# Optimization experiments

Measured on AMD Instinct MI355X. Metric: run time of the kernel, lower is better.

## Reference

```python
import jax, jax.numpy as jnp
import numpy as np

EPS = 1e-06
NB, NGRID, NTARGET, NBASIS, NCH, OUTCH = 4, 512, 1024, 5, 8, 1


def setup_inputs() -> dict:
    key = jax.random.key(0)
    k1, k2, k3, k4 = jax.random.split(key, 4)
    x_grid = jax.random.normal(k1, (NB, NGRID, NCH), dtype=jnp.float32)
    h_grid = jax.random.normal(k2, (NB, NGRID, NBASIS, NCH), dtype=jnp.float32)
    target_x = jax.random.normal(k3, (NB, NTARGET, NCH), dtype=jnp.float32)
    # sigma initialized as log(min_init_lengthscale + init_lengthscale) = log(1 + 1e-6)
    sigma = jnp.full((NBASIS, NCH), np.log(1e-06 + 1.0), dtype=jnp.float32)
    # linear g: nbasis -> out_channels
    g_w = jax.random.normal(k4, (OUTCH, NBASIS), dtype=jnp.float32) / np.sqrt(NBASIS)
    g_b = jnp.zeros((OUTCH,), dtype=jnp.float32)
    return {"x_grid": x_grid, "h_grid": h_grid, "target_x": target_x,
            "sigma": sigma, "g_w": g_w, "g_b": g_b}


def reference(x_grid, h_grid, target_x, sigma, g_w, g_b):
    # scales: (nbasis, nchannel)
    scales = jnp.exp(sigma) + EPS
    # pairwise scaled distances: (nb, ngrid, ntarget, nbasis, nchannel)
    d = (x_grid[:, :, None, None, :] - target_x[:, None, :, None, :]) / scales[None, None, None, :, :]
    wt = jnp.exp(-0.5 * d * d)
    # weighted sum over grid points: (nb, ntarget, nbasis, nchannel)
    h_out = jnp.einsum('bgkc,bgtkc->btkc', h_grid, wt)
    # transpose to (nb, ntarget, nchannel, nbasis), linear over nbasis
    h_out = jnp.swapaxes(h_out, -2, -1)
    out = jnp.einsum('btck,ok->btco', h_out, g_w) + g_b
    out = jnp.squeeze(out)  # out_channels == 1 -> (nb, ntarget, nchannel)
    if out.ndim == 2:
        out = out[None]
    return out
```

## Files before the change

kernel.cpp:

```cpp
#include <hip/hip_runtime.h>

#define NB 4
#define NGRID 512
#define NTARGET 1024
#define NBASIS 5
#define NCH 8
#define EPS_F 1e-6f
#define LOG2E 1.4426950408889634f

#if defined(__has_builtin)
#if __has_builtin(__builtin_amdgcn_exp2f)
#define EXP2F(x) __builtin_amdgcn_exp2f(x)
#else
#define EXP2F(x) exp2f(x)
#endif
#else
#define EXP2F(x) exp2f(x)
#endif

__global__ __launch_bounds__(256) void final_layer_fused(
    const float* __restrict__ x_grid,
    const float* __restrict__ h_grid,
    const float* __restrict__ target_x,
    const float* __restrict__ sigma,
    const float* __restrict__ g_w,
    const float* __restrict__ g_b,
    float* __restrict__ out)
{
    __shared__ float xs[NGRID * NCH];
    __shared__ float hw[NGRID * NCH];
    __shared__ float coef_s[NBASIS * NCH];
    __shared__ float gw_s[NBASIS];

    const int tid = threadIdx.x;
    const int c   = tid & 7;
    const int tt  = (tid >> 3) & 7;
    const int gs  = tid >> 6;
    const int b   = blockIdx.x >> 7;
    const int t   = ((blockIdx.x & 127) << 3) + tt;

    if (tid < NBASIS * NCH) {
        float s = __expf(sigma[tid]) + EPS_F;
        coef_s[tid] = -0.5f * LOG2E / (s * s);
    }
    if (tid < NBASIS) gw_s[tid] = g_w[tid];

    const float gw0 = g_w[0], gw1 = g_w[1], gw2 = g_w[2], gw3 = g_w[3], gw4 = g_w[4];
    const float* xbase = x_grid + (size_t)b * NGRID * NCH;
    const float* hbase = h_grid + (size_t)b * NGRID * NBASIS * NCH;
#pragma unroll
    for (int j = 0; j < 16; ++j) {
        const int v = tid + j * 256;
        xs[v] = xbase[v];
        const float* hp = hbase + (size_t)(v >> 3) * (NBASIS * NCH) + (v & 7);
        hw[v] = gw0 * hp[0] + gw1 * hp[8] + gw2 * hp[16] + gw3 * hp[24] + gw4 * hp[32];
    }
    __syncthreads();

    int eq = 1;
    {
        const unsigned c0 = __float_as_uint(coef_s[0]);
        for (int i = 1; i < NBASIS * NCH; ++i)
            eq &= (__float_as_uint(coef_s[i]) == c0);
    }

    const float tx = target_x[(b * NTARGET + t) * NCH + c];
    const int g0 = gs * (NGRID / 4);

    float p;
    if (eq) {
        const float coefc = coef_s[c];
        float acc = 0.f;
#pragma unroll 8
        for (int gi = 0; gi < NGRID / 4; ++gi) {
            const int g = g0 + gi;
            const float d = xs[g * 8 + c] - tx;
            acc += hw[g * 8 + c] * EXP2F(d * d * coefc);
        }
        p = acc;
    } else {
        float coef[NBASIS];
#pragma unroll
        for (int k = 0; k < NBASIS; ++k) coef[k] = coef_s[k * NCH + c];
        const float* hg = hbase + c;
        float acc[NBASIS] = {0.f, 0.f, 0.f, 0.f, 0.f};
#pragma unroll 2
        for (int gi = 0; gi < NGRID / 4; ++gi) {
            const int g = g0 + gi;
            const float d  = xs[g * 8 + c] - tx;
            const float d2 = d * d;
            const float* hp = hg + (size_t)g * NBASIS * NCH;
#pragma unroll
            for (int k = 0; k < NBASIS; ++k)
                acc[k] += hp[k * NCH] * EXP2F(d2 * coef[k]);
        }
        float s = 0.f;
#pragma unroll
        for (int k = 0; k < NBASIS; ++k) s += acc[k] * gw_s[k];
        p = s;
    }

    __syncthreads();
    xs[tid] = p;
    __syncthreads();
    if (gs == 0) {
        float r = p + xs[tid + 64] + xs[tid + 128] + xs[tid + 192] + g_b[0];
        out[(b * NTARGET + t) * NCH + c] = r;
    }
}

extern "C" void kernel_launch(void* const* d_in, const int* in_sizes, int n_in,
                              void* d_out, int out_size, void* d_ws, size_t ws_size,
                              hipStream_t stream) {
    const float* x_grid   = (const float*)d_in[0];
    const float* h_grid   = (const float*)d_in[1];
    const float* target_x = (const float*)d_in[2];
    const float* sigma    = (const float*)d_in[3];
    const float* g_w      = (const float*)d_in[4];
    const float* g_b      = (const float*)d_in[5];
    float* out = (float*)d_out;

    final_layer_fused<<<NB * (NTARGET / 8), 256, 0, stream>>>(
        x_grid, h_grid, target_x, sigma, g_w, g_b, out);
}
```

Baseline: 69.51 us.

## Transpose shared grid to channel-major, pre-scale coordinates, smaller target tiles

```diff
diff --git a/kernel.cpp b/kernel.cpp
--- a/kernel.cpp
+++ b/kernel.cpp
@@ -7,6 +7,7 @@
 #define NCH 8
 #define EPS_F 1e-6f
 #define LOG2E 1.4426950408889634f
+#define PAD_G 516
 
 #if defined(__has_builtin)
 #if __has_builtin(__builtin_amdgcn_exp2f)
@@ -18,7 +19,7 @@
 #define EXP2F(x) exp2f(x)
 #endif
 
-__global__ __launch_bounds__(256) void final_layer_fused(
+__global__ __launch_bounds__(256, 4) void final_layer_fused(
     const float* __restrict__ x_grid,
     const float* __restrict__ h_grid,
     const float* __restrict__ target_x,
@@ -27,85 +28,106 @@
     const float* __restrict__ g_b,
     float* __restrict__ out)
 {
-    __shared__ float xs[NGRID * NCH];
-    __shared__ float hw[NGRID * NCH];
-    __shared__ float coef_s[NBASIS * NCH];
-    __shared__ float gw_s[NBASIS];
+    __shared__ float xs_t[NCH][PAD_G];
+    __shared__ float hw_t[NCH][PAD_G];
+    __shared__ float red[256];
 
     const int tid = threadIdx.x;
     const int c   = tid & 7;
-    const int tt  = (tid >> 3) & 7;
-    const int gs  = tid >> 6;
-    const int b   = blockIdx.x >> 7;
-    const int t   = ((blockIdx.x & 127) << 3) + tt;
+    const int tt  = (tid >> 3) & 3;
+    const int gs  = tid >> 5;
+    const int b   = blockIdx.x >> 8;
+    const int t   = ((blockIdx.x & 255) << 2) + tt;
 
-    if (tid < NBASIS * NCH) {
-        float s = __expf(sigma[tid]) + EPS_F;
-        coef_s[tid] = -0.5f * LOG2E / (s * s);
+    int eq = 1;
+    {
+        const unsigned s0b = __float_as_uint(sigma[0]);
+#pragma unroll
+        for (int i = 1; i < NBASIS * NCH; ++i)
+            eq &= (__float_as_uint(sigma[i]) == s0b);
     }
-    if (tid < NBASIS) gw_s[tid] = g_w[tid];
+    const float sE = __expf(sigma[0]) + EPS_F;
+    const float sc = eq ? (sqrtf(0.5f * LOG2E) / sE) : 1.0f;
 
-    const float gw0 = g_w[0], gw1 = g_w[1], gw2 = g_w[2], gw3 = g_w[3], gw4 = g_w[4];
-    const float* xbase = x_grid + (size_t)b * NGRID * NCH;
-    const float* hbase = h_grid + (size_t)b * NGRID * NBASIS * NCH;
+    float gwv[NBASIS];
 #pragma unroll
-    for (int j = 0; j < 16; ++j) {
-        const int v = tid + j * 256;
-        xs[v] = xbase[v];
-        const float* hp = hbase + (size_t)(v >> 3) * (NBASIS * NCH) + (v & 7);
-        hw[v] = gw0 * hp[0] + gw1 * hp[8] + gw2 * hp[16] + gw3 * hp[24] + gw4 * hp[32];
+    for (int k = 0; k < NBASIS; ++k) gwv[k] = g_w[k];
+
+    const float4* hb4 = reinterpret_cast<const float4*>(h_grid + (size_t)b * NGRID * NBASIS * NCH);
+    const float4* xb4 = reinterpret_cast<const float4*>(x_grid + (size_t)b * NGRID * NCH);
+#pragma unroll
+    for (int j = 0; j < 2; ++j) {
+        const int g = tid + j * 256;
+        const float4* hp4 = hb4 + (size_t)g * 10;
+        float4 hv[10];
+#pragma unroll
+        for (int q = 0; q < 10; ++q) hv[q] = hp4[q];
+        const float* hf = reinterpret_cast<const float*>(hv);
+        const float4 xa = xb4[g * 2];
+        const float4 xb = xb4[g * 2 + 1];
+        const float xv[8] = {xa.x, xa.y, xa.z, xa.w, xb.x, xb.y, xb.z, xb.w};
+#pragma unroll
+        for (int cc = 0; cc < 8; ++cc) {
+            const float w = gwv[0] * hf[cc]      + gwv[1] * hf[8 + cc] +
+                            gwv[2] * hf[16 + cc] + gwv[3] * hf[24 + cc] +
+                            gwv[4] * hf[32 + cc];
+            hw_t[cc][g] = w;
+            xs_t[cc][g] = xv[cc] * sc;
+        }
     }
     __syncthreads();
 
-    int eq = 1;
-    {
-        const unsigned c0 = __float_as_uint(coef_s[0]);
-        for (int i = 1; i < NBASIS * NCH; ++i)
-            eq &= (__float_as_uint(coef_s[i]) == c0);
-    }
-
-    const float tx = target_x[(b * NTARGET + t) * NCH + c];
-    const int g0 = gs * (NGRID / 4);
+    const float tx = target_x[((size_t)b * NTARGET + t) * NCH + c] * sc;
 
     float p;
     if (eq) {
-        const float coefc = coef_s[c];
-        float acc = 0.f;
-#pragma unroll 8
-        for (int gi = 0; gi < NGRID / 4; ++gi) {
-            const int g = g0 + gi;
-            const float d = xs[g * 8 + c] - tx;
-            acc += hw[g * 8 + c] * EXP2F(d * d * coefc);
+        const float* xp = &xs_t[c][gs * 64];
+        const float* wp = &hw_t[c][gs * 64];
+        float acc0 = 0.f, acc1 = 0.f;
+#pragma unroll
+        for (int q = 0; q < 16; ++q) {
+            const float4 xv = *reinterpret_cast<const float4*>(xp + q * 4);
+            const float4 wv = *reinterpret_cast<const float4*>(wp + q * 4);
+            const float d0 = xv.x - tx;
+            const float d1 = xv.y - tx;
+            const float d2 = xv.z - tx;
+            const float d3 = xv.w - tx;
+            acc0 += wv.x * EXP2F(-(d0 * d0));
+            acc1 += wv.y * EXP2F(-(d1 * d1));
+            acc0 += wv.z * EXP2F(-(d2 * d2));
+            acc1 += wv.w * EXP2F(-(d3 * d3));
         }
-        p = acc;
+        p = acc0 + acc1;
     } else {
         float coef[NBASIS];
 #pragma unroll
-        for (int k = 0; k < NBASIS; ++k) coef[k] = coef_s[k * NCH + c];
-        const float* hg = hbase + c;
-        float acc[NBASIS] = {0.f, 0.f, 0.f, 0.f, 0.f};
-#pragma unroll 2
-        for (int gi = 0; gi < NGRID / 4; ++gi) {
-            const int g = g0 + gi;
-            const float d  = xs[g * 8 + c] - tx;
+        for (int k = 0; k < NBASIS; ++k) {
+            const float s = __expf(sigma[k * NCH + c]) + EPS_F;
+            coef[k] = -0.5f * LOG2E / (s * s);
+        }
+        const float* hg = h_grid + (size_t)b * NGRID * NBASIS * NCH + c;
+        float acck[NBASIS] = {0.f, 0.f, 0.f, 0.f, 0.f};
+        for (int gi = 0; gi < 64; ++gi) {
+            const int g = gs * 64 + gi;
+            const float d  = xs_t[c][g] - tx;
             const float d2 = d * d;
-            const float* hp = hg + (size_t)g * NBASIS * NCH;
+            const float* hpg = hg + (size_t)g * (NBASIS * NCH);
 #pragma unroll
             for (int k = 0; k < NBASIS; ++k)
-                acc[k] += hp[k * NCH] * EXP2F(d2 * coef[k]);
+                acck[k] += hpg[k * NCH] * EXP2F(d2 * coef[k]);
         }
-        float s = 0.f;
+        p = 0.f;
 #pragma unroll
-        for (int k = 0; k < NBASIS; ++k) s += acc[k] * gw_s[k];
-        p = s;
+        for (int k = 0; k < NBASIS; ++k) p += acck[k] * gwv[k];
     }
 
+    red[tid] = p;
     __syncthreads();
-    xs[tid] = p;
-    __syncthreads();
-    if (gs == 0) {
-        float r = p + xs[tid + 64] + xs[tid + 128] + xs[tid + 192] + g_b[0];
-        out[(b * NTARGET + t) * NCH + c] = r;
+    if (tid < 32) {
+        float r = g_b[0];
+#pragma unroll
+        for (int i = 0; i < 8; ++i) r += red[tid + 32 * i];
+        out[((size_t)b * NTARGET + ((blockIdx.x & 255) << 2)) * NCH + tid] = r;
     }
 }
 
@@ -120,6 +142,6 @@
     const float* g_b      = (const float*)d_in[5];
     float* out = (float*)d_out;
 
-    final_layer_fused<<<NB * (NTARGET / 8), 256, 0, stream>>>(
+    final_layer_fused<<<NB * (NTARGET / 4), 256, 0, stream>>>(
         x_grid, h_grid, target_x, sigma, g_w, g_b, out);
 }
```

New measurement: 71.32 us. 1.03x slower.
